# Optimization experiments

Measured on AMD Instinct MI355X. Metric: run time of the kernel, lower is better.

## Reference

```python
import jax, jax.numpy as jnp
import numpy as np

B, H, D = 4096, 1024, 4
SCALE = 20.0
EPS = 1e-7
LABEL_GATE = 0.01


def _layer_norm(x, g, b, eps=1e-5):
    mu = jnp.mean(x, axis=-1, keepdims=True)
    var = jnp.mean(jnp.square(x - mu), axis=-1, keepdims=True)
    return (x - mu) * jax.lax.rsqrt(var + eps) * g + b


def setup_inputs() -> dict:
    key = jax.random.key(0)
    ks = jax.random.split(key, 8)
    s = 0.02
    return {
        "pooled": jax.random.normal(ks[0], (B, H), dtype=jnp.float32),
        "labels": jax.random.uniform(ks[1], (B, D), dtype=jnp.float32),
        "ln1_g": jnp.ones((H,), jnp.float32),
        "ln1_b": jnp.zeros((H,), jnp.float32),
        "W1": jax.random.normal(ks[2], (H, H // 2), dtype=jnp.float32) * s,
        "b1": jnp.zeros((H // 2,), jnp.float32),
        "ln2_g": jnp.ones((H // 2,), jnp.float32),
        "ln2_b": jnp.zeros((H // 2,), jnp.float32),
        "W2": jax.random.normal(ks[3], (H // 2, H // 4), dtype=jnp.float32) * s,
        "b2": jnp.zeros((H // 4,), jnp.float32),
        "Wh": jax.random.normal(ks[4], (H // 4, D), dtype=jnp.float32) * s,
        "bh": jnp.zeros((D,), jnp.float32),
    }


def reference(pooled, labels, ln1_g, ln1_b, W1, b1, ln2_g, ln2_b, W2, b2, Wh, bh):
    # MLP head (dropout = identity in eval mode); exact GELU as in torch nn.GELU
    h1 = jax.nn.gelu(_layer_norm(pooled, ln1_g, ln1_b) @ W1 + b1, approximate=False)
    h2 = jax.nn.gelu(_layer_norm(h1, ln2_g, ln2_b) @ W2 + b2, approximate=False)
    logits = jax.nn.sigmoid(h2 @ Wh + bh)  # [B, D]

    # MSE term
    mse = jnp.mean(jnp.square(logits - labels))

    # Vectorized pairwise ordering loss over all i<j pairs and dims
    ldiff = labels[:, None, :] - labels[None, :, :]   # [B, B, D]
    pdiff = logits[:, None, :] - logits[None, :, :]   # [B, B, D]
    target_prob = jax.nn.sigmoid(SCALE * ldiff)
    pred_prob = jax.nn.sigmoid(SCALE * pdiff)
    bce = -target_prob * jnp.log(pred_prob + EPS) - (1.0 - target_prob) * jnp.log(1.0 - pred_prob + EPS)

    iu = jnp.triu(jnp.ones((B, B), dtype=bool), k=1)[:, :, None]  # i < j
    mask = iu & (jnp.abs(ldiff) > LABEL_GATE)
    cnt = jnp.sum(mask)
    ordering = jnp.where(cnt > 0, jnp.sum(jnp.where(mask, bce, 0.0)) / jnp.maximum(cnt, 1).astype(bce.dtype), 0.0)

    loss = 0.5 * mse + 0.5 * ordering
    return loss, logits
```

## Files before the change

### kernel.cpp

```cpp
#include <hip/hip_runtime.h>
#include <math.h>
#include <stdint.h>

typedef unsigned short u16;
typedef unsigned long long u64;
typedef __attribute__((ext_vector_type(8))) short bf16x8;
typedef __attribute__((ext_vector_type(4))) float f32x4;

#define RSQRT1_2F 0.70710678118654752440f

__device__ __forceinline__ u16 rne_bf16(float x) {
  unsigned u = __float_as_uint(x);
  return (u16)((u + 0x7FFFu + ((u >> 16) & 1u)) >> 16);
}
__device__ __forceinline__ float bf16_to_f(u16 h) {
  return __uint_as_float(((unsigned)h) << 16);
}
__device__ __forceinline__ void gload_lds16(const void* g, void* l) {
  __builtin_amdgcn_global_load_lds(
      (__attribute__((address_space(1))) void*)(uintptr_t)g,
      (__attribute__((address_space(3))) void*)(uintptr_t)l, 16, 0, 0);
}
__device__ __forceinline__ float rlane(float v, int sl) {
  return __uint_as_float((unsigned)__builtin_amdgcn_readlane((int)__float_as_uint(v), sl));
}
__device__ __forceinline__ float block_reduce_sum_f(float v, float* smem4) {
  #pragma unroll
  for (int off = 32; off > 0; off >>= 1) v += __shfl_down(v, off, 64);
  const int lane = threadIdx.x & 63;
  const int wid  = threadIdx.x >> 6;
  if (lane == 0) smem4[wid] = v;
  __syncthreads();
  float r = smem4[0] + smem4[1] + smem4[2] + smem4[3];
  __syncthreads();
  return r;
}
__device__ __forceinline__ float gelu_exact(float z) {
  return 0.5f * z * (1.0f + erff(z * RSQRT1_2F));
}

template<int H, int NPT>
__device__ __forceinline__ void ln_split_body(
    const float* __restrict__ x, const float* __restrict__ g,
    const float* __restrict__ b, u16* __restrict__ yhi, u16* __restrict__ ylo,
    int row, float* smem4) {
  const float* xr = x + (size_t)row * H;
  const int tid = threadIdx.x;
  float v[NPT];
  #pragma unroll
  for (int q = 0; q < NPT; ++q) v[q] = xr[tid + q * 256];
  float s = 0.f;
  #pragma unroll
  for (int q = 0; q < NPT; ++q) s += v[q];
  s = block_reduce_sum_f(s, smem4);
  const float mu = s * (1.0f / H);
  float s2 = 0.f;
  #pragma unroll
  for (int q = 0; q < NPT; ++q) { float d = v[q] - mu; s2 = fmaf(d, d, s2); }
  s2 = block_reduce_sum_f(s2, smem4);
  const float rstd = rsqrtf(s2 * (1.0f / H) + 1e-5f);
  #pragma unroll
  for (int q = 0; q < NPT; ++q) {
    const int c = tid + q * 256;
    const float y = (v[q] - mu) * rstd * g[c] + b[c];
    const u16 h = rne_bf16(y);
    const u16 lo = rne_bf16(y - bf16_to_f(h));
    yhi[(size_t)row * H + c] = h;
    ylo[(size_t)row * H + c] = lo;
  }
}

template<int K, int N>
__device__ __forceinline__ void wsplit_body(
    const float* __restrict__ W, u16* __restrict__ Whi, u16* __restrict__ Wlo,
    int ntile, int ktile, float* sm ) {
  const int t = threadIdx.x;
  const int n0 = ntile * 64, k0 = ktile * 64;
  #pragma unroll
  for (int q = 0; q < 16; ++q) {
    const int r = q * 4 + (t >> 6);
    sm[r * 65 + (t & 63)] = W[(size_t)(k0 + r) * N + n0 + (t & 63)];
  }
  __syncthreads();
  #pragma unroll
  for (int q = 0; q < 16; ++q) {
    const int nr = q * 4 + (t >> 6);
    const int kc = t & 63;
    const float v = sm[kc * 65 + nr];
    const u16 h = rne_bf16(v);
    const u16 lo = rne_bf16(v - bf16_to_f(h));
    Whi[(size_t)(n0 + nr) * K + k0 + kc] = h;
    Wlo[(size_t)(n0 + nr) * K + k0 + kc] = lo;
  }
}

__global__ __launch_bounds__(256) void prep_kernel(
    const float* __restrict__ pooled, const float* __restrict__ ln1_g,
    const float* __restrict__ ln1_b, const float* __restrict__ W1,
    const float* __restrict__ W2,
    u16* __restrict__ xhi, u16* __restrict__ xlo,
    u16* __restrict__ w1thi, u16* __restrict__ w1tlo,
    u16* __restrict__ w2thi, u16* __restrict__ w2tlo) {
  __shared__ float sm[64 * 65];
  const int bid = blockIdx.x;
  if (bid < 4096) {
    ln_split_body<1024, 4>(pooled, ln1_g, ln1_b, xhi, xlo, bid, sm);
  } else if (bid < 4224) {
    const int idx = bid - 4096;
    wsplit_body<1024, 512>(W1, w1thi, w1tlo, idx & 7, idx >> 3, sm);
  } else {
    const int idx = bid - 4224;
    wsplit_body<512, 256>(W2, w2thi, w2tlo, idx & 3, idx >> 2, sm);
  }
}

template<int H, int NPT>
__global__ __launch_bounds__(256) void ln_gelu_split_kernel(
    const float* __restrict__ Pa, const float* __restrict__ Pb,
    const float* __restrict__ bias, const float* __restrict__ g,
    const float* __restrict__ b, u16* __restrict__ yhi, u16* __restrict__ ylo) {
  __shared__ float smem4[4];
  const int row = blockIdx.x;
  const size_t base = (size_t)row * H;
  const int tid = threadIdx.x;
  float v[NPT];
  #pragma unroll
  for (int q = 0; q < NPT; ++q) {
    const int c = tid + q * 256;
    v[q] = gelu_exact(Pa[base + c] + Pb[base + c] + bias[c]);
  }
  float s = 0.f;
  #pragma unroll
  for (int q = 0; q < NPT; ++q) s += v[q];
  s = block_reduce_sum_f(s, smem4);
  const float mu = s * (1.0f / H);
  float s2 = 0.f;
  #pragma unroll
  for (int q = 0; q < NPT; ++q) { float d = v[q] - mu; s2 = fmaf(d, d, s2); }
  s2 = block_reduce_sum_f(s2, smem4);
  const float rstd = rsqrtf(s2 * (1.0f / H) + 1e-5f);
  #pragma unroll
  for (int q = 0; q < NPT; ++q) {
    const int c = tid + q * 256;
    const float y = (v[q] - mu) * rstd * g[c] + b[c];
    const u16 h = rne_bf16(y);
    const u16 lo = rne_bf16(y - bf16_to_f(h));
    yhi[base + c] = h;
    ylo[base + c] = lo;
  }
}

template<int M, int N, int K, int KCH>
__global__ __launch_bounds__(256, 2) void gemm_bf16x3_partial(
    const u16* __restrict__ Ahi, const u16* __restrict__ Alo,
    const u16* __restrict__ Bhi, const u16* __restrict__ Blo,
    float* __restrict__ P, double* zclr) {
  if (zclr && blockIdx.x == 0 && blockIdx.y == 0 && blockIdx.z == 0 &&
      threadIdx.x < 32) {
    zclr[threadIdx.x] = 0.0;
    zclr[32 + threadIdx.x] = 0.0;
    ((u64*)(zclr + 64))[threadIdx.x] = 0ull;
  }
  __shared__ __align__(16) char sb[49152];
  const int t = threadIdx.x;
  const int w = t >> 6;
  const int l = t & 63;
  const int lm = l & 15, lk = l >> 4;
  const int wm = w >> 1, wn = w & 1;

  const int gx = gridDim.x, gy = gridDim.y;
  const int nwg = gx * gy * gridDim.z;
  const int bid = blockIdx.x + gx * (blockIdx.y + gy * blockIdx.z);
  int swz = (bid & 7) * (nwg >> 3) + (bid >> 3);
  const int bx = swz % gx; swz /= gx;
  const int by = swz % gy;
  const int bz = swz / gy;

  const int m0 = by * 128, n0 = bx * 64;
  const int kbase = bz * KCH;
  float* __restrict__ Pz = P + (size_t)bz * M * N;

  f32x4 acc[4][2];
  #pragma unroll
  for (int m = 0; m < 4; ++m)
    #pragma unroll
    for (int n = 0; n < 2; ++n)
      #pragma unroll
      for (int r = 0; r < 4; ++r) acc[m][n][r] = 0.f;

  const int srow = t >> 3;
  const int sslot = (t & 7) * 16;

  for (int k0 = kbase; k0 < kbase + KCH; k0 += 64) {
    #pragma unroll
    for (int q = 0; q < 4; ++q) {
      const int row = q * 32 + srow;
      const int cl = sslot ^ ((row & 7) << 4);
      const size_t gb = ((size_t)(m0 + row) * K + k0) * 2 + cl;
      gload_lds16((const char*)Ahi + gb, sb + q * 4096 + w * 1024);
      gload_lds16((const char*)Alo + gb, sb + 16384 + q * 4096 + w * 1024);
    }
    #pragma unroll
    for (int q = 0; q < 2; ++q) {
      const int row = q * 32 + srow;
      const int cl = sslot ^ ((row & 7) << 4);
      const size_t gb = ((size_t)(n0 + row) * K + k0) * 2 + cl;
      gload_lds16((const char*)Bhi + gb, sb + 32768 + q * 4096 + w * 1024);
      gload_lds16((const char*)Blo + gb, sb + 40960 + q * 4096 + w * 1024);
    }
    __syncthreads();

    #pragma unroll
    for (int kk = 0; kk < 2; ++kk) {
      const int cbase = kk * 64 + lk * 16;
      bf16x8 ah[4], al[4];
      #pragma unroll
      for (int m = 0; m < 4; ++m) {
        const int row = wm * 64 + m * 16 + lm;
        const int c = cbase ^ ((row & 7) << 4);
        ah[m] = *(const bf16x8*)(sb + row * 128 + c);
        al[m] = *(const bf16x8*)(sb + 16384 + row * 128 + c);
      }
      bf16x8 bh[2], bl[2];
      #pragma unroll
      for (int n = 0; n < 2; ++n) {
        const int row = wn * 32 + n * 16 + lm;
        const int c = cbase ^ ((row & 7) << 4);
        bh[n] = *(const bf16x8*)(sb + 32768 + row * 128 + c);
        bl[n] = *(const bf16x8*)(sb + 40960 + row * 128 + c);
      }
      #pragma unroll
      for (int m = 0; m < 4; ++m)
        #pragma unroll
        for (int n = 0; n < 2; ++n) {
          acc[m][n] = __builtin_amdgcn_mfma_f32_16x16x32_bf16(ah[m], bh[n], acc[m][n], 0, 0, 0);
          acc[m][n] = __builtin_amdgcn_mfma_f32_16x16x32_bf16(ah[m], bl[n], acc[m][n], 0, 0, 0);
          acc[m][n] = __builtin_amdgcn_mfma_f32_16x16x32_bf16(al[m], bh[n], acc[m][n], 0, 0, 0);
        }
    }
    __syncthreads();
  }

  #pragma unroll
  for (int m = 0; m < 4; ++m)
    #pragma unroll
    for (int n = 0; n < 2; ++n) {
      const int col = n0 + wn * 32 + n * 16 + lm;
      #pragma unroll
      for (int r = 0; r < 4; ++r) {
        const int row = m0 + wm * 64 + m * 16 + lk * 4 + r;
        Pz[(size_t)row * N + col] = acc[m][n][r];
      }
    }
}

template<int NZ>
__global__ __launch_bounds__(256) void head_kernel(
    const float* __restrict__ P2, const float* __restrict__ b2,
    const float* __restrict__ Wh, const float* __restrict__ bh,
    const float* __restrict__ labels,
    float* __restrict__ logits_out, float* __restrict__ To,
    float* __restrict__ Eo, float* __restrict__ Lo,
    double* __restrict__ mse_slots) {
  const int lane = threadIdx.x & 63;
  const int wv   = threadIdx.x >> 6;
  const int row  = blockIdx.x * 4 + wv;
  const size_t base = (size_t)row * 256;
  constexpr size_t ZSTRIDE = (size_t)4096 * 256;
  float a0 = 0.f, a1 = 0.f, a2 = 0.f, a3 = 0.f;
  #pragma unroll
  for (int q = 0; q < 4; ++q) {
    const int k = lane + q * 64;
    float s = b2[k];
    #pragma unroll
    for (int z = 0; z < NZ; ++z) s += P2[z * ZSTRIDE + base + k];
    const float hv = gelu_exact(s);
    const float4 wv4 = *(const float4*)&Wh[k * 4];
    a0 = fmaf(hv, wv4.x, a0); a1 = fmaf(hv, wv4.y, a1);
    a2 = fmaf(hv, wv4.z, a2); a3 = fmaf(hv, wv4.w, a3);
  }
  #pragma unroll
  for (int off = 32; off > 0; off >>= 1) {
    a0 += __shfl_down(a0, off, 64);
    a1 += __shfl_down(a1, off, 64);
    a2 += __shfl_down(a2, off, 64);
    a3 += __shfl_down(a3, off, 64);
  }
  if (lane == 0) {
    const float z[4] = {a0 + bh[0], a1 + bh[1], a2 + bh[2], a3 + bh[3]};
    float msew = 0.f;
    #pragma unroll
    for (int d = 0; d < 4; ++d) {
      const float p = 1.0f / (1.0f + expf(-z[d]));
      const float lab = labels[row * 4 + d];
      logits_out[row * 4 + d] = p;
      To[row * 4 + d] = 20.0f * p;
      Eo[row * 4 + d] = expf(20.0f * p);
      Lo[row * 4 + d] = expf(20.0f * lab);
      const float df = p - lab;
      msew = fmaf(df, df, msew);
    }
    atomicAdd(&mse_slots[row & 31], (double)msew);
  }
}

#define GFUN(t) ((t) * 64 - (t) * ((t) - 1) / 2)
#define TGATE 0.0498339962f

__global__ __launch_bounds__(256) void pairwise_kernel(
    const float* __restrict__ To, const float* __restrict__ E,
    const float* __restrict__ L, double* __restrict__ slots) {
  const int lane = threadIdx.x & 63;
  const int wv   = threadIdx.x >> 6;
  const int idx  = blockIdx.x * 4 + wv;
  const int tile = idx >> 1;
  const int jbase = (idx & 1) * 32;

  int ti = (int)((129.0f - sqrtf(fmaxf(16641.0f - 8.0f * (float)tile, 0.f))) * 0.5f);
  if (ti < 0) ti = 0; if (ti > 63) ti = 63;
  while (ti > 0 && GFUN(ti) > tile) ti--;
  while (ti < 63 && GFUN(ti + 1) <= tile) ti++;
  const int tj = ti + (tile - GFUN(ti));
  const int i0 = ti * 64, j0 = tj * 64;
  const int i = i0 + lane, j = j0 + lane;

  const float4 e4 = *(const float4*)&E[(size_t)i * 4];
  const float4 t4 = *(const float4*)&To[(size_t)i * 4];
  const float4 l4 = *(const float4*)&L[(size_t)i * 4];
  const float Ei[4] = {e4.x, e4.y, e4.z, e4.w};
  const float Ti[4] = {t4.x, t4.y, t4.z, t4.w};
  const float Li[4] = {l4.x, l4.y, l4.z, l4.w};
  const float4 ej4 = *(const float4*)&E[(size_t)j * 4];
  const float4 tj4 = *(const float4*)&To[(size_t)j * 4];
  const float4 lj4 = *(const float4*)&L[(size_t)j * 4];
  const float Ejv[4] = {ej4.x, ej4.y, ej4.z, ej4.w};
  const float Tjv[4] = {tj4.x, tj4.y, tj4.z, tj4.w};
  const float Ljv[4] = {lj4.x, lj4.y, lj4.z, lj4.w};

  const bool diag = (ti == tj);
  float acc[4] = {0.f, 0.f, 0.f, 0.f};
  int cnt = 0;
  #pragma unroll 8
  for (int s = 0; s < 32; ++s) {
    const int jj = jbase + s;
    const bool jok = !diag || (jj > lane);
    #pragma unroll
    for (int d = 0; d < 4; ++d) {
      const float Ej = rlane(Ejv[d], jj);
      const float Tj = rlane(Tjv[d], jj);
      const float Lj = rlane(Ljv[d], jj);
      const float logse = __logf(Ei[d] + Ej);
      const float tt = Li[d] * __builtin_amdgcn_rcpf(Li[d] + Lj);
      const float bce = (logse - Tj) - tt * (Ti[d] - Tj);
      const bool m = jok && (fabsf(tt - 0.5f) > TGATE);
      acc[d] += m ? bce : 0.f;
      cnt += m ? 1 : 0;
    }
  }

  float tot = (acc[0] + acc[1]) + (acc[2] + acc[3]);
  #pragma unroll
  for (int off = 32; off > 0; off >>= 1) {
    tot += __shfl_down(tot, off, 64);
    cnt += __shfl_down(cnt, off, 64);
  }
  if (lane == 0) {
    const int sl = idx & 31;
    atomicAdd(&slots[32 + sl], (double)tot);
    atomicAdd((u64*)(slots + 64) + sl, (u64)cnt);
  }
}

__global__ void finalize_kernel(const double* __restrict__ slots,
                                float* __restrict__ out) {
  const int l = threadIdx.x;
  double m = (l < 32) ? slots[l] : 0.0;
  double o = (l < 32) ? slots[32 + l] : 0.0;
  double c = (l < 32) ? (double)((const u64*)(slots + 64))[l] : 0.0;
  #pragma unroll
  for (int off = 32; off > 0; off >>= 1) {
    m += __shfl_down(m, off, 64);
    o += __shfl_down(o, off, 64);
    c += __shfl_down(c, off, 64);
  }
  if (l == 0) {
    const double mse = m / (4096.0 * 4.0);
    const double ord = (c > 0.0) ? (o / c) : 0.0;
    out[0] = (float)(0.5 * mse + 0.5 * ord);
  }
}

extern "C" void kernel_launch(void* const* d_in, const int* in_sizes, int n_in,
                              void* d_out, int out_size, void* d_ws, size_t ws_size,
                              hipStream_t stream) {
  const float* pooled = (const float*)d_in[0];
  const float* labels = (const float*)d_in[1];
  const float* ln1_g  = (const float*)d_in[2];
  const float* ln1_b  = (const float*)d_in[3];
  const float* W1     = (const float*)d_in[4];
  const float* b1     = (const float*)d_in[5];
  const float* ln2_g  = (const float*)d_in[6];
  const float* ln2_b  = (const float*)d_in[7];
  const float* W2     = (const float*)d_in[8];
  const float* b2     = (const float*)d_in[9];
  const float* Wh     = (const float*)d_in[10];
  const float* bh     = (const float*)d_in[11];
  float* out = (float*)d_out;

  char* ws = (char*)d_ws;
  u16*   xhi   = (u16*)(ws + 0);
  u16*   xlo   = (u16*)(ws + 8388608);
  u16*   w1thi = (u16*)(ws + 16777216);
  u16*   w1tlo = (u16*)(ws + 17825792);
  float* P1    = (float*)(ws + 18874368);
  u16*   h1nhi = (u16*)(ws + 0);
  u16*   h1nlo = (u16*)(ws + 4194304);
  u16*   w2thi = (u16*)(ws + 8388608);
  u16*   w2tlo = (u16*)(ws + 8650752);
  float* P2    = (float*)(ws + 8912896);
  float* Eo    = (float*)(ws + 25690112);
  float* To    = (float*)(ws + 25755648);
  float* Lo    = (float*)(ws + 25821184);
  double* slots = (double*)(ws + 25886720);

  prep_kernel<<<4256, 256, 0, stream>>>(pooled, ln1_g, ln1_b, W1, W2,
                                        xhi, xlo, w1thi, w1tlo, w2thi, w2tlo);
  gemm_bf16x3_partial<4096, 512, 1024, 512><<<dim3(8, 32, 2), 256, 0, stream>>>(
      xhi, xlo, w1thi, w1tlo, P1, nullptr);
  ln_gelu_split_kernel<512, 2><<<4096, 256, 0, stream>>>(
      P1, P1 + (size_t)4096 * 512, b1, ln2_g, ln2_b, h1nhi, h1nlo);
  gemm_bf16x3_partial<4096, 256, 512, 128><<<dim3(4, 32, 4), 256, 0, stream>>>(
      h1nhi, h1nlo, w2thi, w2tlo, P2, slots);
  head_kernel<4><<<1024, 256, 0, stream>>>(
      P2, b2, Wh, bh, labels, out + 1, To, Eo, Lo, slots);
  pairwise_kernel<<<1040, 256, 0, stream>>>(To, Eo, Lo, slots);
  finalize_kernel<<<1, 64, 0, stream>>>(slots, out);
}
```

Baseline: 190.3 us.

## Replace split-K GEMMs with double-buffered full-K GEMMs fusing bias+GELU epilogue

Both GEMMs drop split-K partial sums and now run the full K in one block. They use smaller M tiles, a 32-wide K step and double-buffered LDS staging so global-to-LDS loads overlap the MFMA work. Bias and exact GELU move into the GEMM epilogue, so the LN2 kernel and head kernel read finished activations instead of summing partials. The pairwise kernel is split into finer 16-column slices across twice as many blocks. The aim is less partial-sum traffic and better latency hiding, at the cost of smaller tiles with less data reuse.

```diff
diff --git a/kernel.cpp b/kernel.cpp
--- a/kernel.cpp
+++ b/kernel.cpp
@@ -114,151 +114,125 @@
   }
 }
 
-template<int H, int NPT>
-__global__ __launch_bounds__(256) void ln_gelu_split_kernel(
-    const float* __restrict__ Pa, const float* __restrict__ Pb,
-    const float* __restrict__ bias, const float* __restrict__ g,
-    const float* __restrict__ b, u16* __restrict__ yhi, u16* __restrict__ ylo) {
-  __shared__ float smem4[4];
-  const int row = blockIdx.x;
-  const size_t base = (size_t)row * H;
-  const int tid = threadIdx.x;
-  float v[NPT];
-  #pragma unroll
-  for (int q = 0; q < NPT; ++q) {
-    const int c = tid + q * 256;
-    v[q] = gelu_exact(Pa[base + c] + Pb[base + c] + bias[c]);
-  }
-  float s = 0.f;
-  #pragma unroll
-  for (int q = 0; q < NPT; ++q) s += v[q];
-  s = block_reduce_sum_f(s, smem4);
-  const float mu = s * (1.0f / H);
-  float s2 = 0.f;
-  #pragma unroll
-  for (int q = 0; q < NPT; ++q) { float d = v[q] - mu; s2 = fmaf(d, d, s2); }
-  s2 = block_reduce_sum_f(s2, smem4);
-  const float rstd = rsqrtf(s2 * (1.0f / H) + 1e-5f);
-  #pragma unroll
-  for (int q = 0; q < NPT; ++q) {
-    const int c = tid + q * 256;
-    const float y = (v[q] - mu) * rstd * g[c] + b[c];
-    const u16 h = rne_bf16(y);
-    const u16 lo = rne_bf16(y - bf16_to_f(h));
-    yhi[base + c] = h;
-    ylo[base + c] = lo;
-  }
-}
-
-template<int M, int N, int K, int KCH>
-__global__ __launch_bounds__(256, 2) void gemm_bf16x3_partial(
+template<int BM, int NX, int MY, int K>
+__global__ __launch_bounds__(256) void gemm_gelu_kernel(
     const u16* __restrict__ Ahi, const u16* __restrict__ Alo,
     const u16* __restrict__ Bhi, const u16* __restrict__ Blo,
-    float* __restrict__ P, double* zclr) {
-  if (zclr && blockIdx.x == 0 && blockIdx.y == 0 && blockIdx.z == 0 &&
-      threadIdx.x < 32) {
+    const float* __restrict__ bias, float* __restrict__ C, double* zclr) {
+  constexpr int N  = NX * 64;
+  constexpr int MF = BM / 32;
+  constexpr int ABYTES = BM * 64;
+  constexpr int AOFF = 2 * ABYTES;
+  constexpr int BUF  = AOFF + 8192;
+  constexpr int NS   = K / 32;
+  __shared__ __align__(16) char sb[2 * BUF];
+
+  if (zclr && blockIdx.x == 0 && threadIdx.x < 32) {
     zclr[threadIdx.x] = 0.0;
     zclr[32 + threadIdx.x] = 0.0;
     ((u64*)(zclr + 64))[threadIdx.x] = 0ull;
   }
-  __shared__ __align__(16) char sb[49152];
-  const int t = threadIdx.x;
-  const int w = t >> 6;
-  const int l = t & 63;
+
+  const int t = threadIdx.x, w = t >> 6, l = t & 63;
   const int lm = l & 15, lk = l >> 4;
   const int wm = w >> 1, wn = w & 1;
-
-  const int gx = gridDim.x, gy = gridDim.y;
-  const int nwg = gx * gy * gridDim.z;
-  const int bid = blockIdx.x + gx * (blockIdx.y + gy * blockIdx.z);
-  int swz = (bid & 7) * (nwg >> 3) + (bid >> 3);
-  const int bx = swz % gx; swz /= gx;
-  const int by = swz % gy;
-  const int bz = swz / gy;
-
-  const int m0 = by * 128, n0 = bx * 64;
-  const int kbase = bz * KCH;
-  float* __restrict__ Pz = P + (size_t)bz * M * N;
-
-  f32x4 acc[4][2];
-  #pragma unroll
-  for (int m = 0; m < 4; ++m)
+  int bid = (int)blockIdx.x;
+  bid = (bid & 7) * ((NX * MY) >> 3) + (bid >> 3);
+  const int my = bid / NX, nx = bid % NX;
+  const int m0 = my * BM, n0 = nx * 64;
+
+  f32x4 acc[MF][2];
+  #pragma unroll
+  for (int m = 0; m < MF; ++m)
     #pragma unroll
     for (int n = 0; n < 2; ++n)
       #pragma unroll
       for (int r = 0; r < 4; ++r) acc[m][n][r] = 0.f;
 
-  const int srow = t >> 3;
-  const int sslot = (t & 7) * 16;
-
-  for (int k0 = kbase; k0 < kbase + KCH; k0 += 64) {
-    #pragma unroll
-    for (int q = 0; q < 4; ++q) {
-      const int row = q * 32 + srow;
-      const int cl = sslot ^ ((row & 7) << 4);
-      const size_t gb = ((size_t)(m0 + row) * K + k0) * 2 + cl;
-      gload_lds16((const char*)Ahi + gb, sb + q * 4096 + w * 1024);
-      gload_lds16((const char*)Alo + gb, sb + 16384 + q * 4096 + w * 1024);
-    }
-    #pragma unroll
-    for (int q = 0; q < 2; ++q) {
-      const int row = q * 32 + srow;
-      const int cl = sslot ^ ((row & 7) << 4);
-      const size_t gb = ((size_t)(n0 + row) * K + k0) * 2 + cl;
-      gload_lds16((const char*)Bhi + gb, sb + 32768 + q * 4096 + w * 1024);
-      gload_lds16((const char*)Blo + gb, sb + 40960 + q * 4096 + w * 1024);
-    }
-    __syncthreads();
-
-    #pragma unroll
-    for (int kk = 0; kk < 2; ++kk) {
-      const int cbase = kk * 64 + lk * 16;
-      bf16x8 ah[4], al[4];
-      #pragma unroll
-      for (int m = 0; m < 4; ++m) {
-        const int row = wm * 64 + m * 16 + lm;
-        const int c = cbase ^ ((row & 7) << 4);
-        ah[m] = *(const bf16x8*)(sb + row * 128 + c);
-        al[m] = *(const bf16x8*)(sb + 16384 + row * 128 + c);
-      }
-      bf16x8 bh[2], bl[2];
+  auto STAGE = [&](int bufsel, int k0) {
+    char* bb = sb + bufsel * BUF;
+    if constexpr (BM == 64) {
+      const int row = t >> 2, cq = (t & 3) * 16;
+      const int col = cq ^ (((row >> 1) & 3) << 4);
+      const size_t gb = ((size_t)(m0 + row) * K + k0) * 2 + col;
+      gload_lds16((const char*)Ahi + gb, bb + t * 16);
+      gload_lds16((const char*)Alo + gb, bb + ABYTES + t * 16);
+    } else {
+      const int half = t >> 7, tt = t & 127;
+      const int row = tt >> 2, cq = (tt & 3) * 16;
+      const int col = cq ^ (((row >> 1) & 3) << 4);
+      const size_t gb = ((size_t)(m0 + row) * K + k0) * 2 + col;
+      gload_lds16((const char*)(half ? Alo : Ahi) + gb,
+                  bb + half * ABYTES + tt * 16);
+    }
+    {
+      const int row = t >> 2, cq = (t & 3) * 16;
+      const int col = cq ^ (((row >> 1) & 3) << 4);
+      const size_t gb = ((size_t)(n0 + row) * K + k0) * 2 + col;
+      gload_lds16((const char*)Bhi + gb, bb + AOFF + t * 16);
+      gload_lds16((const char*)Blo + gb, bb + AOFF + 4096 + t * 16);
+    }
+  };
+  auto COMPUTE = [&](int bufsel) {
+    char* bb = sb + bufsel * BUF;
+    bf16x8 ah[MF], al[MF], bhv[2], blv[2];
+    #pragma unroll
+    for (int m = 0; m < MF; ++m) {
+      const int row = wm * (BM / 2) + m * 16 + lm;
+      const int col = (lk * 16) ^ (((row >> 1) & 3) << 4);
+      ah[m] = *(const bf16x8*)(bb + row * 64 + col);
+      al[m] = *(const bf16x8*)(bb + ABYTES + row * 64 + col);
+    }
+    #pragma unroll
+    for (int n = 0; n < 2; ++n) {
+      const int row = wn * 32 + n * 16 + lm;
+      const int col = (lk * 16) ^ (((row >> 1) & 3) << 4);
+      bhv[n] = *(const bf16x8*)(bb + AOFF + row * 64 + col);
+      blv[n] = *(const bf16x8*)(bb + AOFF + 4096 + row * 64 + col);
+    }
+    #pragma unroll
+    for (int m = 0; m < MF; ++m)
       #pragma unroll
       for (int n = 0; n < 2; ++n) {
-        const int row = wn * 32 + n * 16 + lm;
-        const int c = cbase ^ ((row & 7) << 4);
-        bh[n] = *(const bf16x8*)(sb + 32768 + row * 128 + c);
-        bl[n] = *(const bf16x8*)(sb + 40960 + row * 128 + c);
+        acc[m][n] = __builtin_amdgcn_mfma_f32_16x16x32_bf16(ah[m], bhv[n], acc[m][n], 0, 0, 0);
+        acc[m][n] = __builtin_amdgcn_mfma_f32_16x16x32_bf16(ah[m], blv[n], acc[m][n], 0, 0, 0);
+        acc[m][n] = __builtin_amdgcn_mfma_f32_16x16x32_bf16(al[m], bhv[n], acc[m][n], 0, 0, 0);
       }
-      #pragma unroll
-      for (int m = 0; m < 4; ++m)
-        #pragma unroll
-        for (int n = 0; n < 2; ++n) {
-          acc[m][n] = __builtin_amdgcn_mfma_f32_16x16x32_bf16(ah[m], bh[n], acc[m][n], 0, 0, 0);
-          acc[m][n] = __builtin_amdgcn_mfma_f32_16x16x32_bf16(ah[m], bl[n], acc[m][n], 0, 0, 0);
-          acc[m][n] = __builtin_amdgcn_mfma_f32_16x16x32_bf16(al[m], bh[n], acc[m][n], 0, 0, 0);
-        }
-    }
+  };
+
+  STAGE(0, 0);
+  __syncthreads();
+  for (int s = 0; s < NS; ++s) {
+    if (s + 1 < NS) STAGE((s + 1) & 1, (s + 1) * 32);
+    COMPUTE(s & 1);
     __syncthreads();
   }
 
   #pragma unroll
-  for (int m = 0; m < 4; ++m)
+  for (int m = 0; m < MF; ++m)
     #pragma unroll
     for (int n = 0; n < 2; ++n) {
       const int col = n0 + wn * 32 + n * 16 + lm;
+      const float bv = bias[col];
       #pragma unroll
       for (int r = 0; r < 4; ++r) {
-        const int row = m0 + wm * 64 + m * 16 + lk * 4 + r;
-        Pz[(size_t)row * N + col] = acc[m][n][r];
+        const int row = m0 + wm * (BM / 2) + m * 16 + lk * 4 + r;
+        C[(size_t)row * N + col] = gelu_exact(acc[m][n][r] + bv);
       }
     }
 }
 
-template<int NZ>
+template<int H, int NPT>
+__global__ __launch_bounds__(256) void ln2_kernel(
+    const float* __restrict__ x, const float* __restrict__ g,
+    const float* __restrict__ b, u16* __restrict__ yhi, u16* __restrict__ ylo) {
+  __shared__ float smem4[4];
+  ln_split_body<H, NPT>(x, g, b, yhi, ylo, blockIdx.x, smem4);
+}
+
 __global__ __launch_bounds__(256) void head_kernel(
-    const float* __restrict__ P2, const float* __restrict__ b2,
-    const float* __restrict__ Wh, const float* __restrict__ bh,
-    const float* __restrict__ labels,
+    const float* __restrict__ h2g, const float* __restrict__ Wh,
+    const float* __restrict__ bh, const float* __restrict__ labels,
     float* __restrict__ logits_out, float* __restrict__ To,
     float* __restrict__ Eo, float* __restrict__ Lo,
     double* __restrict__ mse_slots) {
@@ -266,15 +240,11 @@
   const int wv   = threadIdx.x >> 6;
   const int row  = blockIdx.x * 4 + wv;
   const size_t base = (size_t)row * 256;
-  constexpr size_t ZSTRIDE = (size_t)4096 * 256;
   float a0 = 0.f, a1 = 0.f, a2 = 0.f, a3 = 0.f;
   #pragma unroll
   for (int q = 0; q < 4; ++q) {
     const int k = lane + q * 64;
-    float s = b2[k];
-    #pragma unroll
-    for (int z = 0; z < NZ; ++z) s += P2[z * ZSTRIDE + base + k];
-    const float hv = gelu_exact(s);
+    const float hv = h2g[base + k];
     const float4 wv4 = *(const float4*)&Wh[k * 4];
     a0 = fmaf(hv, wv4.x, a0); a1 = fmaf(hv, wv4.y, a1);
     a2 = fmaf(hv, wv4.z, a2); a3 = fmaf(hv, wv4.w, a3);
@@ -313,16 +283,15 @@
   const int lane = threadIdx.x & 63;
   const int wv   = threadIdx.x >> 6;
   const int idx  = blockIdx.x * 4 + wv;
-  const int tile = idx >> 1;
-  const int jbase = (idx & 1) * 32;
+  const int tile = idx >> 2;
+  const int jbase = (idx & 3) * 16;
 
   int ti = (int)((129.0f - sqrtf(fmaxf(16641.0f - 8.0f * (float)tile, 0.f))) * 0.5f);
   if (ti < 0) ti = 0; if (ti > 63) ti = 63;
   while (ti > 0 && GFUN(ti) > tile) ti--;
   while (ti < 63 && GFUN(ti + 1) <= tile) ti++;
   const int tj = ti + (tile - GFUN(ti));
-  const int i0 = ti * 64, j0 = tj * 64;
-  const int i = i0 + lane, j = j0 + lane;
+  const int i = ti * 64 + lane, j = tj * 64 + lane;
 
   const float4 e4 = *(const float4*)&E[(size_t)i * 4];
   const float4 t4 = *(const float4*)&To[(size_t)i * 4];
@@ -340,8 +309,8 @@
   const bool diag = (ti == tj);
   float acc[4] = {0.f, 0.f, 0.f, 0.f};
   int cnt = 0;
-  #pragma unroll 8
-  for (int s = 0; s < 32; ++s) {
+  #pragma unroll
+  for (int s = 0; s < 16; ++s) {
     const int jj = jbase + s;
     const bool jok = !diag || (jj > lane);
     #pragma unroll
@@ -408,31 +377,31 @@
   float* out = (float*)d_out;
 
   char* ws = (char*)d_ws;
+  const size_t MB_ = 1048576;
   u16*   xhi   = (u16*)(ws + 0);
-  u16*   xlo   = (u16*)(ws + 8388608);
-  u16*   w1thi = (u16*)(ws + 16777216);
-  u16*   w1tlo = (u16*)(ws + 17825792);
-  float* P1    = (float*)(ws + 18874368);
-  u16*   h1nhi = (u16*)(ws + 0);
-  u16*   h1nlo = (u16*)(ws + 4194304);
-  u16*   w2thi = (u16*)(ws + 8388608);
-  u16*   w2tlo = (u16*)(ws + 8650752);
-  float* P2    = (float*)(ws + 8912896);
-  float* Eo    = (float*)(ws + 25690112);
-  float* To    = (float*)(ws + 25755648);
-  float* Lo    = (float*)(ws + 25821184);
-  double* slots = (double*)(ws + 25886720);
+  u16*   xlo   = (u16*)(ws + 8 * MB_);
+  u16*   w1thi = (u16*)(ws + 16 * MB_);
+  u16*   w1tlo = (u16*)(ws + 17 * MB_);
+  u16*   w2thi = (u16*)(ws + 18 * MB_);
+  u16*   w2tlo = (u16*)(ws + 18 * MB_ + 262144);
+  float* h1g   = (float*)(ws + 19 * MB_);
+  u16*   h1nhi = (u16*)(ws + 27 * MB_);
+  u16*   h1nlo = (u16*)(ws + 31 * MB_);
+  float* h2g   = (float*)(ws + 35 * MB_);
+  float* Eo    = (float*)(ws + 39 * MB_);
+  float* To    = (float*)(ws + 39 * MB_ + 65536);
+  float* Lo    = (float*)(ws + 39 * MB_ + 131072);
+  double* slots = (double*)(ws + 39 * MB_ + 196608);
 
   prep_kernel<<<4256, 256, 0, stream>>>(pooled, ln1_g, ln1_b, W1, W2,
                                         xhi, xlo, w1thi, w1tlo, w2thi, w2tlo);
-  gemm_bf16x3_partial<4096, 512, 1024, 512><<<dim3(8, 32, 2), 256, 0, stream>>>(
-      xhi, xlo, w1thi, w1tlo, P1, nullptr);
-  ln_gelu_split_kernel<512, 2><<<4096, 256, 0, stream>>>(
-      P1, P1 + (size_t)4096 * 512, b1, ln2_g, ln2_b, h1nhi, h1nlo);
-  gemm_bf16x3_partial<4096, 256, 512, 128><<<dim3(4, 32, 4), 256, 0, stream>>>(
-      h1nhi, h1nlo, w2thi, w2tlo, P2, slots);
-  head_kernel<4><<<1024, 256, 0, stream>>>(
-      P2, b2, Wh, bh, labels, out + 1, To, Eo, Lo, slots);
-  pairwise_kernel<<<1040, 256, 0, stream>>>(To, Eo, Lo, slots);
+  gemm_gelu_kernel<64, 8, 64, 1024><<<512, 256, 0, stream>>>(
+      xhi, xlo, w1thi, w1tlo, b1, h1g, nullptr);
+  ln2_kernel<512, 2><<<4096, 256, 0, stream>>>(h1g, ln2_g, ln2_b, h1nhi, h1nlo);
+  gemm_gelu_kernel<32, 4, 128, 512><<<512, 256, 0, stream>>>(
+      h1nhi, h1nlo, w2thi, w2tlo, b2, h2g, slots);
+  head_kernel<<<1024, 256, 0, stream>>>(
+      h2g, Wh, bh, labels, out + 1, To, Eo, Lo, slots);
+  pairwise_kernel<<<2080, 256, 0, stream>>>(To, Eo, Lo, slots);
   finalize_kernel<<<1, 64, 0, stream>>>(slots, out);
 }
```

New measurement: 213.3 us. +12.1%, slower.
